# Kernel optimization log

Hardware: AMD Instinct MI355X
Metric: run time of the kernel (lower is better)

## Reference

```python
import jax, jax.numpy as jnp
import numpy as np

D_MODEL = 256
N_HEADS_SA = 8
CA_HEADS = 8
CA_DH = 64
CA_INNER = CA_HEADS * CA_DH  # 512
N_POINTS = 4
D_FFN = 1024
OFFSET_SCALE = 2.0
B, NQ = 4, 1024
T, H, W = 4, 64, 64
LV = T * H * W

PNAMES = ['sa_Wq','sa_bq','sa_Wk','sa_bk','sa_Wv','sa_bv','sa_Wo','sa_bo',
          'ln1_g','ln1_b','ln2_g','ln2_b','ln3_g','ln3_b',
          'ca_Wq','ca_bq','ca_Wk','ca_bk','ca_Wv','ca_bv','ca_Wref','ca_bref',
          'ca_Woff','ca_boff','ca_Wo','ca_bo',
          'ffn_W1','ffn_b1','ffn_W2','ffn_b2']


def _layer_norm(x, g, b, eps=1e-5):
    m = x.mean(-1, keepdims=True)
    v = ((x - m) ** 2).mean(-1, keepdims=True)
    return (x - m) * jax.lax.rsqrt(v + eps) * g + b


def _mha(q, k, v, Wq, bq, Wk, bk, Wv, bv, Wo, bo, n_heads):
    Bq, N, D = q.shape
    dh = D // n_heads
    scale = 1.0 / float(np.sqrt(dh))
    qh = (q @ Wq + bq).reshape(Bq, N, n_heads, dh)
    kh = (k @ Wk + bk).reshape(Bq, N, n_heads, dh)
    vh = (v @ Wv + bv).reshape(Bq, N, n_heads, dh)
    attn = jax.nn.softmax(jnp.einsum('bqhd,bkhd->bhqk', qh, kh) * scale, -1)
    out = jnp.einsum('bhqk,bkhd->bqhd', attn, vh).reshape(Bq, N, D)
    return out @ Wo + bo


def _trilinear_sample(vol, loc, sizes_f):
    # vol: [B, L, Hd, dh] flattened (T*H*W) volume per head
    # loc: [B, N, Hd, P, 3] normalized (t, h, w) coords in [0, 1]
    Bv, L, Hd, dh = vol.shape
    _, N, _, P, _ = loc.shape
    pos = jnp.clip(loc, 0.0, 1.0) * (sizes_f - 1.0)  # align_corners voxel coords
    p0 = jnp.floor(pos)
    frac = pos - p0
    p0i = p0.astype(jnp.int32)
    sizes_i = sizes_f.astype(jnp.int32)
    Hn, Wn = sizes_i[1], sizes_i[2]
    vol_t = vol.transpose(0, 2, 1, 3)  # [B, Hd, L, dh]
    out = jnp.zeros((Bv, Hd, N * P, dh), vol.dtype)
    for dt in (0, 1):
        for dy in (0, 1):
            for dx in (0, 1):
                c = jnp.minimum(p0i + jnp.array([dt, dy, dx], jnp.int32), sizes_i - 1)
                wt = (frac[..., 0] if dt else 1.0 - frac[..., 0]) \
                   * (frac[..., 1] if dy else 1.0 - frac[..., 1]) \
                   * (frac[..., 2] if dx else 1.0 - frac[..., 2])  # [B,N,Hd,P]
                idx = c[..., 0] * (Hn * Wn) + c[..., 1] * Wn + c[..., 2]
                idx_t = idx.transpose(0, 2, 1, 3).reshape(Bv, Hd, N * P, 1)
                g = jnp.take_along_axis(vol_t, idx_t, axis=2)  # [B,Hd,N*P,dh]
                w_t = wt.transpose(0, 2, 1, 3).reshape(Bv, Hd, N * P, 1)
                out = out + g * w_t
    return out.reshape(Bv, Hd, N, P, dh).transpose(0, 2, 1, 3, 4)  # [B,N,Hd,P,dh]


def _deform_cross_attn(query, key, value, flow_key, flow_value, spatial_shapes, p):
    Bq, N, _ = query.shape
    L = key.shape[1]
    sizes_f = spatial_shapes[0].astype(jnp.float32)  # single level (T, H, W)
    qh = (query @ p['ca_Wq'] + p['ca_bq']).reshape(Bq, N, CA_HEADS, CA_DH)
    ref = jax.nn.sigmoid(query @ p['ca_Wref'] + p['ca_bref'])  # [B,N,3]
    off = (query @ p['ca_Woff'] + p['ca_boff']).reshape(Bq, N, CA_HEADS, N_POINTS, 3)
    loc = ref[:, :, None, None, :] + off * (OFFSET_SCALE / sizes_f)
    k_vol = (key @ p['ca_Wk'] + p['ca_bk']).reshape(Bq, L, CA_HEADS, CA_DH)
    v_vol = (value @ p['ca_Wv'] + p['ca_bv']).reshape(Bq, L, CA_HEADS, CA_DH)
    fk_vol = (flow_key @ p['ca_Wk'] + p['ca_bk']).reshape(Bq, L, CA_HEADS, CA_DH)
    fv_vol = (flow_value @ p['ca_Wv'] + p['ca_bv']).reshape(Bq, L, CA_HEADS, CA_DH)
    k_s = _trilinear_sample(k_vol, loc, sizes_f)
    v_s = _trilinear_sample(v_vol, loc, sizes_f)
    fk_s = _trilinear_sample(fk_vol, loc, sizes_f)
    fv_s = _trilinear_sample(fv_vol, loc, sizes_f)
    scale = 1.0 / float(np.sqrt(CA_DH))
    logits = jnp.concatenate([
        jnp.einsum('bnhd,bnhpd->bnhp', qh, k_s),
        jnp.einsum('bnhd,bnhpd->bnhp', qh, fk_s)], -1) * scale
    attn = jax.nn.softmax(logits, -1)  # joint softmax over image+flow sampled points
    vals = jnp.concatenate([v_s, fv_s], 3)  # [B,N,Hd,2P,dh]
    out = jnp.einsum('bnhp,bnhpd->bnhd', attn, vals).reshape(Bq, N, CA_INNER)
    return out @ p['ca_Wo'] + p['ca_bo']


def _forward(query, query_pos, img, flow, pos_emb, spatial_shapes, p):
    q = query + query_pos
    sa = _mha(q, q, query, p['sa_Wq'], p['sa_bq'], p['sa_Wk'], p['sa_bk'],
              p['sa_Wv'], p['sa_bv'], p['sa_Wo'], p['sa_bo'], N_HEADS_SA)
    x = _layer_norm(query + sa, p['ln1_g'], p['ln1_b'])
    key = pos_emb + img
    flow_key = pos_emb + flow
    ca = _deform_cross_attn(x, key, img, flow_key, flow, spatial_shapes, p)
    x = _layer_norm(x + ca, p['ln2_g'], p['ln2_b'])
    ffn = jax.nn.relu(x @ p['ffn_W1'] + p['ffn_b1']) @ p['ffn_W2'] + p['ffn_b2']
    return _layer_norm(x + ffn, p['ln3_g'], p['ln3_b'])


def setup_inputs() -> dict:
    key = jax.random.key(0)
    ks = iter(jax.random.split(key, 64))
    def rn(shape, s=1.0):
        return jax.random.normal(next(ks), shape, jnp.float32) * s
    inp = {
        'query': rn((B, NQ, D_MODEL)),
        'query_pos': rn((B, NQ, D_MODEL)),
        'img_embed_flatten': rn((B, LV, D_MODEL)),
        'flow_embed_flatten': rn((B, LV, D_MODEL)),
        'indicator_temporal_lvl_pos_embed_flatten': rn((B, LV, D_MODEL)),
        'spatial_shapes': jnp.array([[T, H, W]], jnp.int32),
    }
    for nm in ['sa_Wq', 'sa_Wk', 'sa_Wv', 'sa_Wo']:
        inp[nm] = rn((D_MODEL, D_MODEL), 0.02)
    for nm in ['sa_bq', 'sa_bk', 'sa_bv', 'sa_bo', 'ln1_b', 'ln2_b', 'ln3_b']:
        inp[nm] = jnp.zeros((D_MODEL,), jnp.float32)
    for nm in ['ln1_g', 'ln2_g', 'ln3_g']:
        inp[nm] = jnp.ones((D_MODEL,), jnp.float32)
    inp['ca_Wq'] = rn((D_MODEL, CA_INNER), 0.02); inp['ca_bq'] = jnp.zeros((CA_INNER,), jnp.float32)
    inp['ca_Wk'] = rn((D_MODEL, CA_INNER), 0.02); inp['ca_bk'] = jnp.zeros((CA_INNER,), jnp.float32)
    inp['ca_Wv'] = rn((D_MODEL, CA_INNER), 0.02); inp['ca_bv'] = jnp.zeros((CA_INNER,), jnp.float32)
    inp['ca_Wref'] = rn((D_MODEL, 3), 0.02); inp['ca_bref'] = jnp.zeros((3,), jnp.float32)
    inp['ca_Woff'] = rn((D_MODEL, CA_HEADS * N_POINTS * 3), 0.02)
    inp['ca_boff'] = jnp.zeros((CA_HEADS * N_POINTS * 3,), jnp.float32)
    inp['ca_Wo'] = rn((CA_INNER, D_MODEL), 0.02); inp['ca_bo'] = jnp.zeros((D_MODEL,), jnp.float32)
    inp['ffn_W1'] = rn((D_MODEL, D_FFN), 0.02); inp['ffn_b1'] = jnp.zeros((D_FFN,), jnp.float32)
    inp['ffn_W2'] = rn((D_FFN, D_MODEL), 0.02); inp['ffn_b2'] = jnp.zeros((D_MODEL,), jnp.float32)
    return inp


def reference(query, query_pos, img_embed_flatten, flow_embed_flatten,
              indicator_temporal_lvl_pos_embed_flatten, spatial_shapes,
              sa_Wq, sa_bq, sa_Wk, sa_bk, sa_Wv, sa_bv, sa_Wo, sa_bo,
              ln1_g, ln1_b, ln2_g, ln2_b, ln3_g, ln3_b,
              ca_Wq, ca_bq, ca_Wk, ca_bk, ca_Wv, ca_bv, ca_Wref, ca_bref,
              ca_Woff, ca_boff, ca_Wo, ca_bo,
              ffn_W1, ffn_b1, ffn_W2, ffn_b2):
    p = dict(zip(PNAMES, (sa_Wq, sa_bq, sa_Wk, sa_bk, sa_Wv, sa_bv, sa_Wo, sa_bo,
                          ln1_g, ln1_b, ln2_g, ln2_b, ln3_g, ln3_b,
                          ca_Wq, ca_bq, ca_Wk, ca_bk, ca_Wv, ca_bv, ca_Wref, ca_bref,
                          ca_Woff, ca_boff, ca_Wo, ca_bo,
                          ffn_W1, ffn_b1, ffn_W2, ffn_b2)))
    return _forward(query, query_pos, img_embed_flatten, flow_embed_flatten,
                    indicator_temporal_lvl_pos_embed_flatten, spatial_shapes, p)
```

## Files before the change

### kernel.cpp

```cpp
#include <hip/hip_runtime.h>
#include <hip/hip_bf16.h>

#define BQ 4
#define NQT 1024
#define DM 256
#define HSA 8
#define DHSA 32
#define CAH 8
#define CADH 64
#define CAI 512
#define NPT 4
#define DFFN 1024
#define TT 4
#define HH 64
#define WW 64
#define LVOL 16384

using bf16 = __hip_bfloat16;
typedef __attribute__((ext_vector_type(4))) float fx4;
typedef __attribute__((ext_vector_type(8))) short s8v;
typedef __attribute__((ext_vector_type(4))) short s4v;

__device__ __forceinline__ float b2f(bf16 v) { return __bfloat162float(v); }
__device__ __forceinline__ bf16  f2b(float v) { return __float2bfloat16(v); }
__device__ __forceinline__ short f2bs(float v) {
  bf16 b = __float2bfloat16(v);
  return *reinterpret_cast<short*>(&b);
}

__device__ __forceinline__ float wave_sum64(float v) {
#pragma unroll
  for (int o = 32; o >= 1; o >>= 1) v += __shfl_xor(v, o, 64);
  return v;
}

__device__ __forceinline__ s8v pack8(float4 a, float4 b) {
  return (s8v){f2bs(a.x), f2bs(a.y), f2bs(a.z), f2bs(a.w),
               f2bs(b.x), f2bs(b.y), f2bs(b.z), f2bs(b.w)};
}

template <int KSH>
__global__ __launch_bounds__(256) void wtrans_k(const float* __restrict__ W,
                                               short* __restrict__ Wt, int N) {
  const int i = blockIdx.x * 256 + threadIdx.x;
  const int k = i & ((1 << KSH) - 1);
  const int n = i >> KSH;
  Wt[i] = f2bs(W[(size_t)k * N + n]);
}

template <int DUAL, int RELU, int OUTBF>
__global__ __launch_bounds__(256) void mgemm_k(
    const float* __restrict__ A, const float* __restrict__ A2,
    const short* __restrict__ Wt, const float* __restrict__ bias,
    void* __restrict__ Cout, int M, int N, int K) {
  __shared__ short As[128 * 40];
  __shared__ short Bs[128 * 40];
  const int tid = threadIdx.x;
  const int lane = tid & 63, w = tid >> 6;
  const int wr = w >> 1, wc = w & 1;
  const int lm = lane & 15, quad = lane >> 4;
  const int m0 = blockIdx.y * 128, n0 = blockIdx.x * 128;
  fx4 acc[4][4] = {};
  for (int k0 = 0; k0 < K; k0 += 32) {
#pragma unroll
    for (int i = 0; i < 4; i++) {
      int m = (tid >> 3) + i * 32;
      int k = (tid & 7) * 4;
      const float4 av = *(const float4*)&A[(size_t)(m0 + m) * K + k0 + k];
      float x0 = av.x, x1 = av.y, x2 = av.z, x3 = av.w;
      if (DUAL) {
        const float4 a2 = *(const float4*)&A2[(size_t)(m0 + m) * K + k0 + k];
        x0 += a2.x; x1 += a2.y; x2 += a2.z; x3 += a2.w;
      }
      s4v sv = {f2bs(x0), f2bs(x1), f2bs(x2), f2bs(x3)};
      *(s4v*)&As[m * 40 + k] = sv;
    }
#pragma unroll
    for (int i = 0; i < 2; i++) {
      int unit = tid + i * 256;
      int n = unit >> 2, c = unit & 3;
      s8v bv = *(const s8v*)&Wt[(size_t)(n0 + n) * K + k0 + c * 8];
      *(s8v*)&Bs[n * 40 + c * 8] = bv;
    }
    __syncthreads();
    s8v af[4], bfr[4];
#pragma unroll
    for (int f = 0; f < 4; f++) {
      af[f] = *(s8v*)&As[(wr * 64 + f * 16 + lm) * 40 + quad * 8];
      bfr[f] = *(s8v*)&Bs[(wc * 64 + f * 16 + lm) * 40 + quad * 8];
    }
#pragma unroll
    for (int fm = 0; fm < 4; fm++)
#pragma unroll
      for (int fn = 0; fn < 4; fn++)
        acc[fm][fn] = __builtin_amdgcn_mfma_f32_16x16x32_bf16(
            af[fm], bfr[fn], acc[fm][fn], 0, 0, 0);
    __syncthreads();
  }
#pragma unroll
  for (int fn = 0; fn < 4; fn++) {
    const int n = n0 + wc * 64 + fn * 16 + lm;
    const float bb = bias[n];
#pragma unroll
    for (int fm = 0; fm < 4; fm++) {
      const int mbase = m0 + wr * 64 + fm * 16 + quad * 4;
#pragma unroll
      for (int r = 0; r < 4; r++) {
        float v = acc[fm][fn][r] + bb;
        if (RELU) v = fmaxf(v, 0.0f);
        const size_t off = (size_t)(mbase + r) * N + n;
        if (OUTBF)
          ((bf16*)Cout)[off] = f2b(v);
        else
          ((float*)Cout)[off] = v;
      }
    }
  }
}

__global__ __launch_bounds__(256) void sa_flash_k(
    const float* __restrict__ qh, const float* __restrict__ kh,
    const float* __restrict__ vh, float* __restrict__ outp) {
  __shared__ short Ks[64 * 72];
  __shared__ short Vt[32 * 72];
  __shared__ short Ps[64 * 72];
  const int qt = blockIdx.x, h = blockIdx.y, b = blockIdx.z;
  const int tid = threadIdx.x;
  const int w = tid >> 6, lane = tid & 63;
  const int lm = lane & 15, quad = lane >> 4;
  const size_t rowbase = (size_t)(b * NQT) * DM + h * DHSA;

  s8v aq;
  {
    const int qrow = qt * 64 + w * 16 + lm;
    const float* qp = &qh[rowbase + (size_t)qrow * DM + quad * 8];
    const float4 q0 = *(const float4*)qp;
    const float4 q1 = *(const float4*)(qp + 4);
    const float sc = 0.17677669529663687f;
    aq = (s8v){f2bs(q0.x * sc), f2bs(q0.y * sc), f2bs(q0.z * sc), f2bs(q0.w * sc),
               f2bs(q1.x * sc), f2bs(q1.y * sc), f2bs(q1.z * sc), f2bs(q1.w * sc)};
  }

  fx4 o0 = {}, o1 = {};
  float mrun[4] = {-1e30f, -1e30f, -1e30f, -1e30f};
  float lrun[4] = {0.f, 0.f, 0.f, 0.f};
  const int jr = tid >> 2;
  const int d0 = (tid & 3) * 8;

  for (int jt = 0; jt < 16; jt++) {
    __syncthreads();
    {
      const size_t rb = rowbase + (size_t)(jt * 64 + jr) * DM + d0;
      const float4 k0 = *(const float4*)&kh[rb];
      const float4 k1 = *(const float4*)&kh[rb + 4];
      *(s8v*)&Ks[jr * 72 + d0] = pack8(k0, k1);
      const float4 v0 = *(const float4*)&vh[rb];
      const float4 v1 = *(const float4*)&vh[rb + 4];
      Vt[(d0 + 0) * 72 + jr] = f2bs(v0.x);
      Vt[(d0 + 1) * 72 + jr] = f2bs(v0.y);
      Vt[(d0 + 2) * 72 + jr] = f2bs(v0.z);
      Vt[(d0 + 3) * 72 + jr] = f2bs(v0.w);
      Vt[(d0 + 4) * 72 + jr] = f2bs(v1.x);
      Vt[(d0 + 5) * 72 + jr] = f2bs(v1.y);
      Vt[(d0 + 6) * 72 + jr] = f2bs(v1.z);
      Vt[(d0 + 7) * 72 + jr] = f2bs(v1.w);
    }
    __syncthreads();
    fx4 s[4];
    const fx4 zero = {};
#pragma unroll
    for (int nf = 0; nf < 4; nf++) {
      s8v kb = *(const s8v*)&Ks[(nf * 16 + lm) * 72 + quad * 8];
      s[nf] = __builtin_amdgcn_mfma_f32_16x16x32_bf16(aq, kb, zero, 0, 0, 0);
    }
#pragma unroll
    for (int r = 0; r < 4; r++) {
      float mx = fmaxf(fmaxf(s[0][r], s[1][r]), fmaxf(s[2][r], s[3][r]));
#pragma unroll
      for (int off = 8; off >= 1; off >>= 1)
        mx = fmaxf(mx, __shfl_xor(mx, off, 64));
      const float mnew = fmaxf(mrun[r], mx);
      const float corr = expf(mrun[r] - mnew);
      mrun[r] = mnew;
      float p0 = expf(s[0][r] - mnew);
      float p1 = expf(s[1][r] - mnew);
      float p2 = expf(s[2][r] - mnew);
      float p3 = expf(s[3][r] - mnew);
      float rs = p0 + p1 + p2 + p3;
#pragma unroll
      for (int off = 8; off >= 1; off >>= 1) rs += __shfl_xor(rs, off, 64);
      lrun[r] = lrun[r] * corr + rs;
      o0[r] *= corr;
      o1[r] *= corr;
      s[0][r] = p0; s[1][r] = p1; s[2][r] = p2; s[3][r] = p3;
    }
#pragma unroll
    for (int nf = 0; nf < 4; nf++)
#pragma unroll
      for (int r = 0; r < 4; r++)
        Ps[(w * 16 + quad * 4 + r) * 72 + nf * 16 + lm] = f2bs(s[nf][r]);
#pragma unroll
    for (int ks = 0; ks < 2; ks++) {
      s8v pf = *(const s8v*)&Ps[(w * 16 + lm) * 72 + ks * 32 + quad * 8];
      s8v vb0 = *(const s8v*)&Vt[lm * 72 + ks * 32 + quad * 8];
      s8v vb1 = *(const s8v*)&Vt[(16 + lm) * 72 + ks * 32 + quad * 8];
      o0 = __builtin_amdgcn_mfma_f32_16x16x32_bf16(pf, vb0, o0, 0, 0, 0);
      o1 = __builtin_amdgcn_mfma_f32_16x16x32_bf16(pf, vb1, o1, 0, 0, 0);
    }
  }
#pragma unroll
  for (int r = 0; r < 4; r++) {
    const float inv = 1.0f / lrun[r];
    const size_t base =
        rowbase + (size_t)(qt * 64 + w * 16 + quad * 4 + r) * DM;
    outp[base + lm] = o0[r] * inv;
    outp[base + 16 + lm] = o1[r] * inv;
  }
}

__global__ __launch_bounds__(128) void refoff_k(
    const float* __restrict__ x1, const float* __restrict__ Wref,
    const float* __restrict__ bref, const float* __restrict__ Woff,
    const float* __restrict__ boff, float* __restrict__ refb,
    float* __restrict__ offb) {
  __shared__ float xs[256];
  const int row = blockIdx.x;
  const int tid = threadIdx.x;
  xs[tid] = x1[(size_t)row * DM + tid];
  xs[tid + 128] = x1[(size_t)row * DM + tid + 128];
  __syncthreads();
  if (tid < 3) {
    float s = bref[tid];
    for (int d = 0; d < 256; d++) s = fmaf(xs[d], Wref[d * 3 + tid], s);
    refb[(size_t)row * 3 + tid] = 1.0f / (1.0f + expf(-s));
  } else if (tid < 99) {
    int o = tid - 3;
    float s = boff[o];
    for (int d = 0; d < 256; d++) s = fmaf(xs[d], Woff[d * 96 + o], s);
    offb[(size_t)row * 96 + o] = s;
  }
}

__device__ __forceinline__ void calc_corners(
    const float* __restrict__ refb, const float* __restrict__ offb, int bn,
    int h, int (&idxs)[NPT][8], float (&wts)[NPT][8]) {
  const float rt = refb[bn * 3 + 0], ry = refb[bn * 3 + 1], rx = refb[bn * 3 + 2];
  const float* ofp = &offb[(size_t)bn * 96 + h * 12];
#pragma unroll
  for (int p = 0; p < NPT; p++) {
    float lt = rt + ofp[p * 3 + 0] * 0.5f;
    float ly = ry + ofp[p * 3 + 1] * 0.03125f;
    float lx = rx + ofp[p * 3 + 2] * 0.03125f;
    float pt = fminf(fmaxf(lt, 0.f), 1.f) * (TT - 1);
    float py = fminf(fmaxf(ly, 0.f), 1.f) * (HH - 1);
    float px = fminf(fmaxf(lx, 0.f), 1.f) * (WW - 1);
    float f0t = floorf(pt), f0y = floorf(py), f0x = floorf(px);
    float frt = pt - f0t, fry = py - f0y, frx = px - f0x;
    int t0 = (int)f0t, y0 = (int)f0y, x0 = (int)f0x;
    int t1 = min(t0 + 1, TT - 1), y1 = min(y0 + 1, HH - 1), x1 = min(x0 + 1, WW - 1);
    float wt0 = 1.f - frt, wy0 = 1.f - fry, wx0 = 1.f - frx;
#pragma unroll
    for (int c = 0; c < 8; c++) {
      int dt = c >> 2, dy = (c >> 1) & 1, dx = c & 1;
      int ct = dt ? t1 : t0, cy = dy ? y1 : y0, cx = dx ? x1 : x0;
      idxs[p][c] = ct * (HH * WW) + cy * WW + cx;
      wts[p][c] = (dt ? frt : wt0) * (dy ? fry : wy0) * (dx ? frx : wx0);
    }
  }
}

__global__ __launch_bounds__(256) void ca_logits_k(
    const float* __restrict__ qh, const float* __restrict__ refb,
    const float* __restrict__ offb, const bf16* __restrict__ vol,
    float* __restrict__ logits, int slot) {
  const int wid = (blockIdx.x * blockDim.x + threadIdx.x) >> 6;
  const int lane = threadIdx.x & 63;
  const int h = wid & 7;
  const int bn = wid >> 3;
  const int b = bn >> 10;
  const float q = qh[(size_t)bn * CAI + h * CADH + lane];
  int idxs[NPT][8];
  float wts[NPT][8];
  calc_corners(refb, offb, bn, h, idxs, wts);
  const size_t volbase = (size_t)b * LVOL * CAI + h * CADH + lane;
  float* lp = logits + ((size_t)bn * CAH + h) * 8 + slot;
#pragma unroll
  for (int p = 0; p < NPT; p++) {
    float ks = 0.f;
#pragma unroll
    for (int c = 0; c < 8; c++)
      ks = fmaf(wts[p][c], b2f(vol[volbase + (size_t)idxs[p][c] * CAI]), ks);
    float li = wave_sum64(q * ks) * 0.125f;
    if (lane == p) lp[p] = li;
  }
}

__global__ __launch_bounds__(256) void ca_softmax_k(float* __restrict__ logits) {
  const int i = blockIdx.x * blockDim.x + threadIdx.x;
  float* p = logits + (size_t)i * 8;
  float v[8], m = -1e30f;
#pragma unroll
  for (int j = 0; j < 8; j++) { v[j] = p[j]; m = fmaxf(m, v[j]); }
  float s = 0.f;
#pragma unroll
  for (int j = 0; j < 8; j++) { v[j] = expf(v[j] - m); s += v[j]; }
  const float inv = 1.0f / s;
#pragma unroll
  for (int j = 0; j < 8; j++) p[j] = v[j] * inv;
}

template <int FIRST>
__global__ __launch_bounds__(256) void ca_acc_k(
    const float* __restrict__ refb, const float* __restrict__ offb,
    const bf16* __restrict__ vol, const float* __restrict__ attn,
    float* __restrict__ acc, int slot) {
  const int wid = (blockIdx.x * blockDim.x + threadIdx.x) >> 6;
  const int lane = threadIdx.x & 63;
  const int h = wid & 7;
  const int bn = wid >> 3;
  const int b = bn >> 10;
  int idxs[NPT][8];
  float wts[NPT][8];
  calc_corners(refb, offb, bn, h, idxs, wts);
  const size_t volbase = (size_t)b * LVOL * CAI + h * CADH + lane;
  const float* ap = attn + ((size_t)bn * CAH + h) * 8 + slot;
  const size_t off = (size_t)bn * CAI + h * CADH + lane;
  float a = FIRST ? 0.f : acc[off];
#pragma unroll
  for (int p = 0; p < NPT; p++) {
    float vs = 0.f;
#pragma unroll
    for (int c = 0; c < 8; c++)
      vs = fmaf(wts[p][c], b2f(vol[volbase + (size_t)idxs[p][c] * CAI]), vs);
    a = fmaf(ap[p], vs, a);
  }
  acc[off] = a;
}

__global__ __launch_bounds__(256) void ln_k(
    const float* __restrict__ resv, const float* __restrict__ x,
    const float* __restrict__ g, const float* __restrict__ bb,
    float* __restrict__ of) {
  const int row = (blockIdx.x * blockDim.x + threadIdx.x) >> 6;
  const int lane = threadIdx.x & 63;
  const size_t base = (size_t)row * DM;
  float v[4];
#pragma unroll
  for (int i = 0; i < 4; i++) {
    int d = lane + i * 64;
    v[i] = resv[base + d] + x[base + d];
  }
  float s = wave_sum64(v[0] + v[1] + v[2] + v[3]);
  const float mean = s * (1.0f / 256.0f);
  float vs = 0.f;
#pragma unroll
  for (int i = 0; i < 4; i++) { float d0 = v[i] - mean; vs = fmaf(d0, d0, vs); }
  vs = wave_sum64(vs);
  const float rstd = rsqrtf(vs * (1.0f / 256.0f) + 1e-5f);
#pragma unroll
  for (int i = 0; i < 4; i++) {
    int d = lane + i * 64;
    of[base + d] = (v[i] - mean) * rstd * g[d] + bb[d];
  }
}

extern "C" void kernel_launch(void* const* d_in, const int* in_sizes, int n_in,
                              void* d_out, int out_size, void* d_ws,
                              size_t ws_size, hipStream_t stream) {
  const float* query = (const float*)d_in[0];
  const float* qpos = (const float*)d_in[1];
  const float* img = (const float*)d_in[2];
  const float* flow = (const float*)d_in[3];
  const float* pos = (const float*)d_in[4];
  const float* sa_Wq = (const float*)d_in[6];
  const float* sa_Wk = (const float*)d_in[7];
  const float* sa_Wv = (const float*)d_in[8];
  const float* sa_Wo = (const float*)d_in[9];
  const float* sa_bq = (const float*)d_in[10];
  const float* sa_bk = (const float*)d_in[11];
  const float* sa_bv = (const float*)d_in[12];
  const float* sa_bo = (const float*)d_in[13];
  const float* ln1_b = (const float*)d_in[14];
  const float* ln2_b = (const float*)d_in[15];
  const float* ln3_b = (const float*)d_in[16];
  const float* ln1_g = (const float*)d_in[17];
  const float* ln2_g = (const float*)d_in[18];
  const float* ln3_g = (const float*)d_in[19];
  const float* ca_Wq = (const float*)d_in[20];
  const float* ca_bq = (const float*)d_in[21];
  const float* ca_Wk = (const float*)d_in[22];
  const float* ca_bk = (const float*)d_in[23];
  const float* ca_Wv = (const float*)d_in[24];
  const float* ca_bv = (const float*)d_in[25];
  const float* ca_Wref = (const float*)d_in[26];
  const float* ca_bref = (const float*)d_in[27];
  const float* ca_Woff = (const float*)d_in[28];
  const float* ca_boff = (const float*)d_in[29];
  const float* ca_Wo = (const float*)d_in[30];
  const float* ca_bo = (const float*)d_in[31];
  const float* ffn_W1 = (const float*)d_in[32];
  const float* ffn_b1 = (const float*)d_in[33];
  const float* ffn_W2 = (const float*)d_in[34];
  const float* ffn_b2 = (const float*)d_in[35];

  const int MQ = BQ * NQT;
  const int MV = BQ * LVOL;
  const size_t MB = 1024 * 1024;

  char* r0 = (char*)d_ws;
  char* w = r0 + 64 * MB;
  auto alloc = [&](size_t n) {
    char* p = w;
    w += (n + 255) & ~(size_t)255;
    return p;
  };
  float* x1_f = (float*)alloc((size_t)MQ * DM * 4);
  float* ca_qh = (float*)alloc((size_t)MQ * CAI * 4);
  float* refb = (float*)alloc((size_t)MQ * 3 * 4);
  float* offb = (float*)alloc((size_t)MQ * 96 * 4);
  float* logits = (float*)alloc((size_t)MQ * CAH * 8 * 4);
  float* ca_acc = (float*)alloc((size_t)MQ * CAI * 4);
  short* WtsaQ = (short*)alloc((size_t)DM * DM * 2);
  short* WtsaK = (short*)alloc((size_t)DM * DM * 2);
  short* WtsaV = (short*)alloc((size_t)DM * DM * 2);
  short* WtsaO = (short*)alloc((size_t)DM * DM * 2);
  short* Wtcaq = (short*)alloc((size_t)CAI * DM * 2);
  short* Wtk = (short*)alloc((size_t)CAI * DM * 2);
  short* Wtv = (short*)alloc((size_t)CAI * DM * 2);
  short* Wtcao = (short*)alloc((size_t)DM * CAI * 2);
  short* Wtf1 = (short*)alloc((size_t)DFFN * DM * 2);
  short* Wtf2 = (short*)alloc((size_t)DM * DFFN * 2);
  if ((size_t)(w - (char*)d_ws) > ws_size) return;

  float* qh_sa = (float*)(r0 + 0 * MB);
  float* kh_sa = (float*)(r0 + 4 * MB);
  float* vh_sa = (float*)(r0 + 8 * MB);
  float* sa_att = (float*)(r0 + 12 * MB);
  float* sa_proj = (float*)(r0 + 16 * MB);
  bf16* vol = (bf16*)r0;
  float* ca_o = (float*)(r0 + 0 * MB);
  float* x2_f = (float*)(r0 + 4 * MB);
  float* ffn_h = (float*)(r0 + 8 * MB);
  float* ffn_o = (float*)(r0 + 24 * MB);

  dim3 blk(256);
  wtrans_k<8><<<dim3(DM * DM / 256), blk, 0, stream>>>(sa_Wq, WtsaQ, DM);
  wtrans_k<8><<<dim3(DM * DM / 256), blk, 0, stream>>>(sa_Wk, WtsaK, DM);
  wtrans_k<8><<<dim3(DM * DM / 256), blk, 0, stream>>>(sa_Wv, WtsaV, DM);
  wtrans_k<8><<<dim3(DM * DM / 256), blk, 0, stream>>>(sa_Wo, WtsaO, DM);
  wtrans_k<8><<<dim3(DM * CAI / 256), blk, 0, stream>>>(ca_Wq, Wtcaq, CAI);
  wtrans_k<8><<<dim3(DM * CAI / 256), blk, 0, stream>>>(ca_Wk, Wtk, CAI);
  wtrans_k<8><<<dim3(DM * CAI / 256), blk, 0, stream>>>(ca_Wv, Wtv, CAI);
  wtrans_k<8><<<dim3(DM * DFFN / 256), blk, 0, stream>>>(ffn_W1, Wtf1, DFFN);
  wtrans_k<9><<<dim3(CAI * DM / 256), blk, 0, stream>>>(ca_Wo, Wtcao, DM);
  wtrans_k<10><<<dim3(DFFN * DM / 256), blk, 0, stream>>>(ffn_W2, Wtf2, DM);
  mgemm_k<1, 0, 0><<<dim3(DM / 128, MQ / 128), blk, 0, stream>>>(query, qpos, WtsaQ, sa_bq, (void*)qh_sa, MQ, DM, DM);
  mgemm_k<1, 0, 0><<<dim3(DM / 128, MQ / 128), blk, 0, stream>>>(query, qpos, WtsaK, sa_bk, (void*)kh_sa, MQ, DM, DM);
  mgemm_k<0, 0, 0><<<dim3(DM / 128, MQ / 128), blk, 0, stream>>>(query, query, WtsaV, sa_bv, (void*)vh_sa, MQ, DM, DM);
  sa_flash_k<<<dim3(16, 8, 4), blk, 0, stream>>>(qh_sa, kh_sa, vh_sa, sa_att);
  mgemm_k<0, 0, 0><<<dim3(DM / 128, MQ / 128), blk, 0, stream>>>(sa_att, sa_att, WtsaO, sa_bo, (void*)sa_proj, MQ, DM, DM);
  ln_k<<<dim3(MQ / 4), blk, 0, stream>>>(query, sa_proj, ln1_g, ln1_b, x1_f);
  mgemm_k<0, 0, 0><<<dim3(CAI / 128, MQ / 128), blk, 0, stream>>>(x1_f, x1_f, Wtcaq, ca_bq, (void*)ca_qh, MQ, CAI, DM);
  refoff_k<<<dim3(MQ), dim3(128), 0, stream>>>(x1_f, ca_Wref, ca_bref, ca_Woff, ca_boff, refb, offb);
  mgemm_k<1, 0, 1><<<dim3(CAI / 128, MV / 128), blk, 0, stream>>>(pos, img, Wtk, ca_bk, (void*)vol, MV, CAI, DM);
  ca_logits_k<<<dim3(8192), blk, 0, stream>>>(ca_qh, refb, offb, vol, logits, 0);
  mgemm_k<1, 0, 1><<<dim3(CAI / 128, MV / 128), blk, 0, stream>>>(pos, flow, Wtk, ca_bk, (void*)vol, MV, CAI, DM);
  ca_logits_k<<<dim3(8192), blk, 0, stream>>>(ca_qh, refb, offb, vol, logits, 4);
  ca_softmax_k<<<dim3(128), blk, 0, stream>>>(logits);
  mgemm_k<0, 0, 1><<<dim3(CAI / 128, MV / 128), blk, 0, stream>>>(img, img, Wtv, ca_bv, (void*)vol, MV, CAI, DM);
  ca_acc_k<1><<<dim3(8192), blk, 0, stream>>>(refb, offb, vol, logits, ca_acc, 0);
  mgemm_k<0, 0, 1><<<dim3(CAI / 128, MV / 128), blk, 0, stream>>>(flow, flow, Wtv, ca_bv, (void*)vol, MV, CAI, DM);
  ca_acc_k<0><<<dim3(8192), blk, 0, stream>>>(refb, offb, vol, logits, ca_acc, 4);
  mgemm_k<0, 0, 0><<<dim3(DM / 128, MQ / 128), blk, 0, stream>>>(ca_acc, ca_acc, Wtcao, ca_bo, (void*)ca_o, MQ, DM, CAI);
  ln_k<<<dim3(MQ / 4), blk, 0, stream>>>(x1_f, ca_o, ln2_g, ln2_b, x2_f);
  mgemm_k<0, 1, 0><<<dim3(DFFN / 128, MQ / 128), blk, 0, stream>>>(x2_f, x2_f, Wtf1, ffn_b1, (void*)ffn_h, MQ, DFFN, DM);
  mgemm_k<0, 0, 0><<<dim3(DM / 128, MQ / 128), blk, 0, stream>>>(ffn_h, ffn_h, Wtf2, ffn_b2, (void*)ffn_o, MQ, DM, DFFN);
  ln_k<<<dim3(MQ / 4), blk, 0, stream>>>(x2_f, ffn_o, ln3_g, ln3_b, (float*)d_out);
}
```

Baseline: 825.6 us.

## Double-buffer GEMM tiles with register prefetch and remap workgroup order

The MFMA GEMM kernel now prefetches the next K-slice of A and W into registers while the current slice is consumed from one of two LDS buffers. This cuts one barrier per iteration and hides global load latency behind the MFMA work. It also remaps block indices so consecutive workgroups spread across an interleaved tile order, which may help L2 or XCD locality. The cost is doubled LDS use and more live registers, which may lower occupancy.

```diff
diff --git a/kernel.cpp b/kernel.cpp
--- a/kernel.cpp
+++ b/kernel.cpp
@@ -53,41 +53,64 @@
     const float* __restrict__ A, const float* __restrict__ A2,
     const short* __restrict__ Wt, const float* __restrict__ bias,
     void* __restrict__ Cout, int M, int N, int K) {
-  __shared__ short As[128 * 40];
-  __shared__ short Bs[128 * 40];
+  __shared__ short As[2][128 * 40];
+  __shared__ short Bs[2][128 * 40];
   const int tid = threadIdx.x;
   const int lane = tid & 63, w = tid >> 6;
   const int wr = w >> 1, wc = w & 1;
   const int lm = lane & 15, quad = lane >> 4;
-  const int m0 = blockIdx.y * 128, n0 = blockIdx.x * 128;
-  fx4 acc[4][4] = {};
-  for (int k0 = 0; k0 < K; k0 += 32) {
+  const int nwg = gridDim.x * gridDim.y;
+  const int ib = blockIdx.y * gridDim.x + blockIdx.x;
+  const int id = (ib & 7) * (nwg >> 3) + (ib >> 3);
+  const int m0 = (id / gridDim.x) * 128;
+  const int n0 = (id % gridDim.x) * 128;
+
+  const int am = tid >> 3, ak = (tid & 7) * 4;
+
+  float4 pa[4], pa2[4];
+  s8v pb[2];
+  auto loadT = [&](int k0) {
 #pragma unroll
     for (int i = 0; i < 4; i++) {
-      int m = (tid >> 3) + i * 32;
-      int k = (tid & 7) * 4;
-      const float4 av = *(const float4*)&A[(size_t)(m0 + m) * K + k0 + k];
-      float x0 = av.x, x1 = av.y, x2 = av.z, x3 = av.w;
-      if (DUAL) {
-        const float4 a2 = *(const float4*)&A2[(size_t)(m0 + m) * K + k0 + k];
-        x0 += a2.x; x1 += a2.y; x2 += a2.z; x3 += a2.w;
-      }
-      s4v sv = {f2bs(x0), f2bs(x1), f2bs(x2), f2bs(x3)};
-      *(s4v*)&As[m * 40 + k] = sv;
+      pa[i] = *(const float4*)&A[(size_t)(m0 + am + i * 32) * K + k0 + ak];
+      if (DUAL)
+        pa2[i] = *(const float4*)&A2[(size_t)(m0 + am + i * 32) * K + k0 + ak];
     }
 #pragma unroll
     for (int i = 0; i < 2; i++) {
       int unit = tid + i * 256;
-      int n = unit >> 2, c = unit & 3;
-      s8v bv = *(const s8v*)&Wt[(size_t)(n0 + n) * K + k0 + c * 8];
-      *(s8v*)&Bs[n * 40 + c * 8] = bv;
-    }
-    __syncthreads();
+      pb[i] = *(const s8v*)&Wt[(size_t)(n0 + (unit >> 2)) * K + k0 +
+                               (unit & 3) * 8];
+    }
+  };
+  auto stageT = [&](int buf) {
+#pragma unroll
+    for (int i = 0; i < 4; i++) {
+      float x0 = pa[i].x, x1 = pa[i].y, x2 = pa[i].z, x3 = pa[i].w;
+      if (DUAL) { x0 += pa2[i].x; x1 += pa2[i].y; x2 += pa2[i].z; x3 += pa2[i].w; }
+      s4v sv = {f2bs(x0), f2bs(x1), f2bs(x2), f2bs(x3)};
+      *(s4v*)&As[buf][(am + i * 32) * 40 + ak] = sv;
+    }
+#pragma unroll
+    for (int i = 0; i < 2; i++) {
+      int unit = tid + i * 256;
+      *(s8v*)&Bs[buf][(unit >> 2) * 40 + (unit & 3) * 8] = pb[i];
+    }
+  };
+
+  fx4 acc[4][4] = {};
+  loadT(0);
+  stageT(0);
+  __syncthreads();
+  int cur = 0;
+  for (int k0 = 0; k0 < K; k0 += 32) {
+    const int more = (k0 + 32 < K);
+    if (more) loadT(k0 + 32);
     s8v af[4], bfr[4];
 #pragma unroll
     for (int f = 0; f < 4; f++) {
-      af[f] = *(s8v*)&As[(wr * 64 + f * 16 + lm) * 40 + quad * 8];
-      bfr[f] = *(s8v*)&Bs[(wc * 64 + f * 16 + lm) * 40 + quad * 8];
+      af[f] = *(s8v*)&As[cur][(wr * 64 + f * 16 + lm) * 40 + quad * 8];
+      bfr[f] = *(s8v*)&Bs[cur][(wc * 64 + f * 16 + lm) * 40 + quad * 8];
     }
 #pragma unroll
     for (int fm = 0; fm < 4; fm++)
@@ -95,7 +118,9 @@
       for (int fn = 0; fn < 4; fn++)
         acc[fm][fn] = __builtin_amdgcn_mfma_f32_16x16x32_bf16(
             af[fm], bfr[fn], acc[fm][fn], 0, 0, 0);
+    if (more) stageT(cur ^ 1);
     __syncthreads();
+    cur ^= 1;
   }
 #pragma unroll
   for (int fn = 0; fn < 4; fn++) {
```

After: 744.6 us. 1.11x faster.

## Double-buffer GEMM LDS tiles with register prefetch, 512 threads, and block swizzle

Applied to the files above, without the earlier changes.

Rewrites the shared MFMA GEMM to use two LDS buffers and prefetch the next K-slices into registers while computing the current one. Each barrier is a plain s_barrier after an LDS wait, so global loads stay in flight across it. Blocks grow to 512 threads (8 waves, 32x64 per wave), and the block index is remapped across groups of 8 to spread tiles. The aim is to hide global load latency and raise occupancy, in exchange for more registers and LDS and a tricky manual schedule.

```diff
diff --git a/kernel.cpp b/kernel.cpp
--- a/kernel.cpp
+++ b/kernel.cpp
@@ -48,62 +48,102 @@
   Wt[i] = f2bs(W[(size_t)k * N + n]);
 }
 
+#define GBAR()                                          \
+  {                                                     \
+    asm volatile("s_waitcnt lgkmcnt(0)" ::: "memory");  \
+    __builtin_amdgcn_sched_barrier(0);                  \
+    __builtin_amdgcn_s_barrier();                       \
+  }
+
+#define LOADSET(S, k0)                                                       \
+  {                                                                          \
+    pa0##S = *(const float4*)&A[(size_t)(m0 + ar) * K + (k0) + ac];          \
+    pa1##S = *(const float4*)&A[(size_t)(m0 + ar + 64) * K + (k0) + ac];     \
+    if (DUAL) {                                                              \
+      qa0##S = *(const float4*)&A2[(size_t)(m0 + ar) * K + (k0) + ac];       \
+      qa1##S = *(const float4*)&A2[(size_t)(m0 + ar + 64) * K + (k0) + ac];  \
+    }                                                                        \
+    pb##S = *(const s8v*)&Wt[(size_t)(n0 + bn) * K + (k0) + bc];             \
+  }
+
+#define STAGESET(S, buf)                                                     \
+  {                                                                          \
+    float4 u = pa0##S;                                                       \
+    if (DUAL) { u.x += qa0##S.x; u.y += qa0##S.y; u.z += qa0##S.z; u.w += qa0##S.w; } \
+    *(s4v*)&As[buf][ar * 40 + ac] =                                          \
+        (s4v){f2bs(u.x), f2bs(u.y), f2bs(u.z), f2bs(u.w)};                   \
+    u = pa1##S;                                                              \
+    if (DUAL) { u.x += qa1##S.x; u.y += qa1##S.y; u.z += qa1##S.z; u.w += qa1##S.w; } \
+    *(s4v*)&As[buf][(ar + 64) * 40 + ac] =                                   \
+        (s4v){f2bs(u.x), f2bs(u.y), f2bs(u.z), f2bs(u.w)};                   \
+    *(s8v*)&Bs[buf][bn * 40 + bc] = pb##S;                                   \
+  }
+
+#define COMPUTE(buf)                                                         \
+  {                                                                          \
+    s8v af[2], bfr[4];                                                       \
+    _Pragma("unroll")                                                        \
+    for (int f = 0; f < 2; f++)                                              \
+      af[f] = *(s8v*)&As[buf][(wr * 32 + f * 16 + lm) * 40 + quad * 8];      \
+    _Pragma("unroll")                                                        \
+    for (int f = 0; f < 4; f++)                                              \
+      bfr[f] = *(s8v*)&Bs[buf][(wc * 64 + f * 16 + lm) * 40 + quad * 8];     \
+    _Pragma("unroll")                                                        \
+    for (int fm = 0; fm < 2; fm++)                                           \
+      _Pragma("unroll")                                                      \
+      for (int fn = 0; fn < 4; fn++)                                         \
+        acc[fm][fn] = __builtin_amdgcn_mfma_f32_16x16x32_bf16(               \
+            af[fm], bfr[fn], acc[fm][fn], 0, 0, 0);                          \
+  }
+
 template <int DUAL, int RELU, int OUTBF>
-__global__ __launch_bounds__(256) void mgemm_k(
+__global__ __launch_bounds__(512, 4) void mgemm_k(
     const float* __restrict__ A, const float* __restrict__ A2,
     const short* __restrict__ Wt, const float* __restrict__ bias,
     void* __restrict__ Cout, int M, int N, int K) {
-  __shared__ short As[128 * 40];
-  __shared__ short Bs[128 * 40];
+  __shared__ short As[2][128 * 40];
+  __shared__ short Bs[2][128 * 40];
   const int tid = threadIdx.x;
   const int lane = tid & 63, w = tid >> 6;
-  const int wr = w >> 1, wc = w & 1;
+  const int wr = w & 3, wc = w >> 2;
   const int lm = lane & 15, quad = lane >> 4;
-  const int m0 = blockIdx.y * 128, n0 = blockIdx.x * 128;
-  fx4 acc[4][4] = {};
-  for (int k0 = 0; k0 < K; k0 += 32) {
-#pragma unroll
-    for (int i = 0; i < 4; i++) {
-      int m = (tid >> 3) + i * 32;
-      int k = (tid & 7) * 4;
-      const float4 av = *(const float4*)&A[(size_t)(m0 + m) * K + k0 + k];
-      float x0 = av.x, x1 = av.y, x2 = av.z, x3 = av.w;
-      if (DUAL) {
-        const float4 a2 = *(const float4*)&A2[(size_t)(m0 + m) * K + k0 + k];
-        x0 += a2.x; x1 += a2.y; x2 += a2.z; x3 += a2.w;
-      }
-      s4v sv = {f2bs(x0), f2bs(x1), f2bs(x2), f2bs(x3)};
-      *(s4v*)&As[m * 40 + k] = sv;
-    }
-#pragma unroll
-    for (int i = 0; i < 2; i++) {
-      int unit = tid + i * 256;
-      int n = unit >> 2, c = unit & 3;
-      s8v bv = *(const s8v*)&Wt[(size_t)(n0 + n) * K + k0 + c * 8];
-      *(s8v*)&Bs[n * 40 + c * 8] = bv;
-    }
-    __syncthreads();
-    s8v af[4], bfr[4];
-#pragma unroll
-    for (int f = 0; f < 4; f++) {
-      af[f] = *(s8v*)&As[(wr * 64 + f * 16 + lm) * 40 + quad * 8];
-      bfr[f] = *(s8v*)&Bs[(wc * 64 + f * 16 + lm) * 40 + quad * 8];
-    }
-#pragma unroll
-    for (int fm = 0; fm < 4; fm++)
-#pragma unroll
-      for (int fn = 0; fn < 4; fn++)
-        acc[fm][fn] = __builtin_amdgcn_mfma_f32_16x16x32_bf16(
-            af[fm], bfr[fn], acc[fm][fn], 0, 0, 0);
-    __syncthreads();
+  const int nwg = gridDim.x * gridDim.y;
+  const int ib = blockIdx.y * gridDim.x + blockIdx.x;
+  const int id = (ib & 7) * (nwg >> 3) + (ib >> 3);
+  const int m0 = (id / gridDim.x) * 128;
+  const int n0 = (id % gridDim.x) * 128;
+
+  const int ar = tid >> 3, ac = (tid & 7) * 4;
+  const int bn = tid >> 2, bc = (tid & 3) * 8;
+
+  float4 pa0A, pa1A, qa0A, qa1A; s8v pbA;
+  float4 pa0B, pa1B, qa0B, qa1B; s8v pbB;
+
+  fx4 acc[2][4] = {};
+  LOADSET(A, 0)
+  LOADSET(B, 32)
+  STAGESET(A, 0)
+  GBAR()
+  int cur = 0;
+  for (int k0 = 0; k0 < K; k0 += 64) {
+    if (k0 + 64 < K) LOADSET(A, k0 + 64)
+    COMPUTE(cur)
+    STAGESET(B, cur ^ 1)
+    GBAR()
+    if (k0 + 96 < K) LOADSET(B, k0 + 96)
+    COMPUTE(cur ^ 1)
+    if (k0 + 64 < K) {
+      STAGESET(A, cur)
+      GBAR()
+    }
   }
 #pragma unroll
   for (int fn = 0; fn < 4; fn++) {
     const int n = n0 + wc * 64 + fn * 16 + lm;
     const float bb = bias[n];
 #pragma unroll
-    for (int fm = 0; fm < 4; fm++) {
-      const int mbase = m0 + wr * 64 + fm * 16 + quad * 4;
+    for (int fm = 0; fm < 2; fm++) {
+      const int mbase = m0 + wr * 32 + fm * 16 + quad * 4;
 #pragma unroll
       for (int r = 0; r < 4; r++) {
         float v = acc[fm][fn][r] + bb;
@@ -444,6 +484,7 @@
   float* ffn_o = (float*)(r0 + 24 * MB);
 
   dim3 blk(256);
+  dim3 blkg(512);
   wtrans_k<8><<<dim3(DM * DM / 256), blk, 0, stream>>>(sa_Wq, WtsaQ, DM);
   wtrans_k<8><<<dim3(DM * DM / 256), blk, 0, stream>>>(sa_Wk, WtsaK, DM);
   wtrans_k<8><<<dim3(DM * DM / 256), blk, 0, stream>>>(sa_Wv, WtsaV, DM);
@@ -454,26 +495,26 @@
   wtrans_k<8><<<dim3(DM * DFFN / 256), blk, 0, stream>>>(ffn_W1, Wtf1, DFFN);
   wtrans_k<9><<<dim3(CAI * DM / 256), blk, 0, stream>>>(ca_Wo, Wtcao, DM);
   wtrans_k<10><<<dim3(DFFN * DM / 256), blk, 0, stream>>>(ffn_W2, Wtf2, DM);
-  mgemm_k<1, 0, 0><<<dim3(DM / 128, MQ / 128), blk, 0, stream>>>(query, qpos, WtsaQ, sa_bq, (void*)qh_sa, MQ, DM, DM);
-  mgemm_k<1, 0, 0><<<dim3(DM / 128, MQ / 128), blk, 0, stream>>>(query, qpos, WtsaK, sa_bk, (void*)kh_sa, MQ, DM, DM);
-  mgemm_k<0, 0, 0><<<dim3(DM / 128, MQ / 128), blk, 0, stream>>>(query, query, WtsaV, sa_bv, (void*)vh_sa, MQ, DM, DM);
+  mgemm_k<1, 0, 0><<<dim3(DM / 128, MQ / 128), blkg, 0, stream>>>(query, qpos, WtsaQ, sa_bq, (void*)qh_sa, MQ, DM, DM);
+  mgemm_k<1, 0, 0><<<dim3(DM / 128, MQ / 128), blkg, 0, stream>>>(query, qpos, WtsaK, sa_bk, (void*)kh_sa, MQ, DM, DM);
+  mgemm_k<0, 0, 0><<<dim3(DM / 128, MQ / 128), blkg, 0, stream>>>(query, query, WtsaV, sa_bv, (void*)vh_sa, MQ, DM, DM);
   sa_flash_k<<<dim3(16, 8, 4), blk, 0, stream>>>(qh_sa, kh_sa, vh_sa, sa_att);
-  mgemm_k<0, 0, 0><<<dim3(DM / 128, MQ / 128), blk, 0, stream>>>(sa_att, sa_att, WtsaO, sa_bo, (void*)sa_proj, MQ, DM, DM);
+  mgemm_k<0, 0, 0><<<dim3(DM / 128, MQ / 128), blkg, 0, stream>>>(sa_att, sa_att, WtsaO, sa_bo, (void*)sa_proj, MQ, DM, DM);
   ln_k<<<dim3(MQ / 4), blk, 0, stream>>>(query, sa_proj, ln1_g, ln1_b, x1_f);
-  mgemm_k<0, 0, 0><<<dim3(CAI / 128, MQ / 128), blk, 0, stream>>>(x1_f, x1_f, Wtcaq, ca_bq, (void*)ca_qh, MQ, CAI, DM);
+  mgemm_k<0, 0, 0><<<dim3(CAI / 128, MQ / 128), blkg, 0, stream>>>(x1_f, x1_f, Wtcaq, ca_bq, (void*)ca_qh, MQ, CAI, DM);
   refoff_k<<<dim3(MQ), dim3(128), 0, stream>>>(x1_f, ca_Wref, ca_bref, ca_Woff, ca_boff, refb, offb);
-  mgemm_k<1, 0, 1><<<dim3(CAI / 128, MV / 128), blk, 0, stream>>>(pos, img, Wtk, ca_bk, (void*)vol, MV, CAI, DM);
+  mgemm_k<1, 0, 1><<<dim3(CAI / 128, MV / 128), blkg, 0, stream>>>(pos, img, Wtk, ca_bk, (void*)vol, MV, CAI, DM);
   ca_logits_k<<<dim3(8192), blk, 0, stream>>>(ca_qh, refb, offb, vol, logits, 0);
-  mgemm_k<1, 0, 1><<<dim3(CAI / 128, MV / 128), blk, 0, stream>>>(pos, flow, Wtk, ca_bk, (void*)vol, MV, CAI, DM);
+  mgemm_k<1, 0, 1><<<dim3(CAI / 128, MV / 128), blkg, 0, stream>>>(pos, flow, Wtk, ca_bk, (void*)vol, MV, CAI, DM);
   ca_logits_k<<<dim3(8192), blk, 0, stream>>>(ca_qh, refb, offb, vol, logits, 4);
   ca_softmax_k<<<dim3(128), blk, 0, stream>>>(logits);
-  mgemm_k<0, 0, 1><<<dim3(CAI / 128, MV / 128), blk, 0, stream>>>(img, img, Wtv, ca_bv, (void*)vol, MV, CAI, DM);
+  mgemm_k<0, 0, 1><<<dim3(CAI / 128, MV / 128), blkg, 0, stream>>>(img, img, Wtv, ca_bv, (void*)vol, MV, CAI, DM);
   ca_acc_k<1><<<dim3(8192), blk, 0, stream>>>(refb, offb, vol, logits, ca_acc, 0);
-  mgemm_k<0, 0, 1><<<dim3(CAI / 128, MV / 128), blk, 0, stream>>>(flow, flow, Wtv, ca_bv, (void*)vol, MV, CAI, DM);
+  mgemm_k<0, 0, 1><<<dim3(CAI / 128, MV / 128), blkg, 0, stream>>>(flow, flow, Wtv, ca_bv, (void*)vol, MV, CAI, DM);
   ca_acc_k<0><<<dim3(8192), blk, 0, stream>>>(refb, offb, vol, logits, ca_acc, 4);
-  mgemm_k<0, 0, 0><<<dim3(DM / 128, MQ / 128), blk, 0, stream>>>(ca_acc, ca_acc, Wtcao, ca_bo, (void*)ca_o, MQ, DM, CAI);
+  mgemm_k<0, 0, 0><<<dim3(DM / 128, MQ / 128), blkg, 0, stream>>>(ca_acc, ca_acc, Wtcao, ca_bo, (void*)ca_o, MQ, DM, CAI);
   ln_k<<<dim3(MQ / 4), blk, 0, stream>>>(x1_f, ca_o, ln2_g, ln2_b, x2_f);
-  mgemm_k<0, 1, 0><<<dim3(DFFN / 128, MQ / 128), blk, 0, stream>>>(x2_f, x2_f, Wtf1, ffn_b1, (void*)ffn_h, MQ, DFFN, DM);
-  mgemm_k<0, 0, 0><<<dim3(DM / 128, MQ / 128), blk, 0, stream>>>(ffn_h, ffn_h, Wtf2, ffn_b2, (void*)ffn_o, MQ, DM, DFFN);
+  mgemm_k<0, 1, 0><<<dim3(DFFN / 128, MQ / 128), blkg, 0, stream>>>(x2_f, x2_f, Wtf1, ffn_b1, (void*)ffn_h, MQ, DFFN, DM);
+  mgemm_k<0, 0, 0><<<dim3(DM / 128, MQ / 128), blkg, 0, stream>>>(ffn_h, ffn_h, Wtf2, ffn_b2, (void*)ffn_o, MQ, DM, DFFN);
   ln_k<<<dim3(MQ / 4), blk, 0, stream>>>(x2_f, ffn_o, ln3_g, ln3_b, (float*)d_out);
 }
```

Measured after the change: 764.4 us. -7.4%, faster.
